# Optimization experiments

Measured on AMD Instinct MI355X. Metric: run time of the kernel, lower is better.

## Reference

```python
import jax, jax.numpy as jnp
import numpy as np

NUM_GENES = 50000
NUM_EDGES = 5000
NNZ = 1_600_000
NUM_PATHWAYS = 500
NUM_TREATMENTS = 20
D = 128        # embed_dim
LATENT = 128   # latent_dim
B, M = 64, 200


def setup_inputs() -> dict:
    key = jax.random.key(0)
    ks = jax.random.split(key, 14)
    gene_ids = jax.random.randint(ks[0], (B, M), 0, NUM_GENES)
    context_ids = jax.random.randint(ks[1], (B,), 0, NUM_TREATMENTS)
    # sparse incidence H (COO): H[row, col] = val, shape [NUM_GENES, NUM_EDGES]
    H_rows = jax.random.randint(ks[2], (NNZ,), 0, NUM_GENES)
    H_cols = jax.random.randint(ks[3], (NNZ,), 0, NUM_EDGES)
    H_vals = jnp.ones((NNZ,), jnp.float32)
    gene_embed = 0.02 * jax.random.normal(ks[4], (NUM_GENES, D), jnp.float32)
    treatment_embed = 0.02 * jax.random.normal(ks[5], (NUM_TREATMENTS, D), jnp.float32)
    gene_pathway = jax.random.bernoulli(ks[6], 0.05, (NUM_GENES, NUM_PATHWAYS)).astype(jnp.float32)
    s = 1.0 / np.sqrt(2 * D)
    W1 = s * jax.random.normal(ks[7], (2 * D, D), jnp.float32)
    b1 = jnp.zeros((D,), jnp.float32)
    W2 = (1.0 / np.sqrt(D)) * jax.random.normal(ks[8], (D,), jnp.float32)
    b2 = jnp.zeros((), jnp.float32)
    latent_W = (1.0 / np.sqrt(D)) * jax.random.normal(ks[9], (D, LATENT), jnp.float32)
    latent_b = jnp.zeros((LATENT,), jnp.float32)
    risk_W = (1.0 / np.sqrt(LATENT)) * jax.random.normal(ks[10], (LATENT,), jnp.float32)
    risk_b = jnp.zeros((), jnp.float32)
    return dict(gene_ids=gene_ids, context_ids=context_ids, H_rows=H_rows, H_cols=H_cols,
                H_vals=H_vals, gene_embed=gene_embed, treatment_embed=treatment_embed,
                gene_pathway=gene_pathway, W1=W1, b1=b1, W2=W2, b2=b2,
                latent_W=latent_W, latent_b=latent_b, risk_W=risk_W, risk_b=risk_b)


def _hyper_prop(E, H_rows, H_cols, H_vals):
    Dv = jax.ops.segment_sum(H_vals, H_rows, num_segments=NUM_GENES)
    De = jax.ops.segment_sum(H_vals, H_cols, num_segments=NUM_EDGES)
    dv = jnp.power(Dv + 1e-6, -0.5)[:, None]   # [V,1]
    de = jnp.power(De + 1e-6, -1.0)[:, None]   # [E,1]
    X = E * dv
    # H^T X : scatter node rows into hyperedges
    HX = jax.ops.segment_sum(H_vals[:, None] * X[H_rows], H_cols, num_segments=NUM_EDGES)
    HX = HX * de
    # H (De^-1 H^T X)
    Xp = jax.ops.segment_sum(H_vals[:, None] * HX[H_cols], H_rows, num_segments=NUM_GENES)
    return Xp * dv


def reference(gene_ids, context_ids, H_rows, H_cols, H_vals, gene_embed, treatment_embed,
              gene_pathway, W1, b1, W2, b2, latent_W, latent_b, risk_W, risk_b):
    E_prop = _hyper_prop(gene_embed, H_rows, H_cols, H_vals)   # [V,D]
    X = E_prop[gene_ids]                                       # [B,M,D]
    ctx = treatment_embed[context_ids]                         # [B,D]
    masks = gene_pathway[gene_ids]                             # [B,M,P]
    pathway_sum = jnp.einsum('bmd,bmp->bpd', X, masks)         # [B,P,D]
    counts = jnp.clip(masks.sum(axis=1), 1.0)[..., None]       # [B,P,1]
    rep = pathway_sum / counts                                 # [B,P,D]
    ctx_exp = jnp.broadcast_to(ctx[:, None, :], (rep.shape[0], NUM_PATHWAYS, D))
    attn_in = jnp.concatenate([rep, ctx_exp], axis=-1)         # [B,P,2D]
    h = jnp.tanh(attn_in @ W1 + b1)                            # [B,P,D]
    scores = h @ W2 + b2                                       # [B,P]
    w = jax.nn.softmax(scores, axis=-1)
    z0 = jnp.einsum('bp,bpd->bd', w, rep)                      # [B,D]
    z = z0 @ latent_W + latent_b                               # [B,LATENT]
    risk = z @ risk_W + risk_b                                 # [B]
    return risk, z
```

## Files before the change

kernel.cpp:

```cpp
#include <hip/hip_runtime.h>
#include <math.h>

#define NGENES 50000
#define NEDGES 5000
#define NNZ_C 1600000
#define NPATH 500
#define DIM 128
#define BB 64
#define MM 200
#define BMN (BB * MM)
#define NBMW 1568
#define CSRCAP 400000
#define NCH 128
#define CHUNK (NNZ_C / NCH)
#define RNG 12512
#define GSTRIDE 50048
#define NT 8
#define TILESZ 6250
#define NBIN (NT * NEDGES)
#define BIN0 50048
#define RED_N 90048
#define SCB_BIN 40
#define SCB_ROW 49
#define SCB (SCB_BIN + SCB_ROW)


__device__ inline float wred_sum(float x) {
#pragma unroll
  for (int off = 32; off > 0; off >>= 1) x += __shfl_down(x, off, 64);
  return x;
}
__device__ inline int wred_sumi(int x) {
#pragma unroll
  for (int off = 32; off > 0; off >>= 1) x += __shfl_down(x, off, 64);
  return x;
}
__device__ inline float wred_max(float x) {
#pragma unroll
  for (int off = 32; off > 0; off >>= 1) x = fmaxf(x, __shfl_down(x, off, 64));
  return x;
}
__device__ inline int wave_incl_scan(int x) {
  int lane = threadIdx.x & 63;
#pragma unroll
  for (int off = 1; off < 64; off <<= 1) {
    int y = __shfl_up(x, off, 64);
    if (lane >= off) x += y;
  }
  return x;
}

__global__ void k_mark(const int* __restrict__ gene_ids, unsigned* __restrict__ bitmap) {
  int i = blockIdx.x * blockDim.x + threadIdx.x;
  if (i >= BMN) return;
  int g = gene_ids[i];
  atomicOr(bitmap + (g >> 5), 1u << (g & 31));
}

__global__ void k_build(const int* __restrict__ rows, const int* __restrict__ cols,
                        unsigned char* __restrict__ pgc, unsigned char* __restrict__ pbc) {
  __shared__ int hs[RNG];
  int c = blockIdx.x, role = blockIdx.y, tid = threadIdx.x;
  int lo = c * CHUNK, hi = lo + CHUNK;
  if (role == 0) {
    for (int j = tid; j < RNG; j += 1024) hs[j] = 0;
    __syncthreads();
    for (int i = lo + tid; i < hi; i += 1024) {
      int r = rows[i];
      int k = r / RNG;
      int j = r - k * RNG;
      atomicAdd(&hs[j], 1 << (k * 8));
    }
    __syncthreads();
    unsigned char* dst = pgc + (size_t)c * GSTRIDE;
    for (int j = tid; j < RNG; j += 1024) {
      unsigned v = (unsigned)hs[j];
      dst[j] = (unsigned char)(v & 0xFFu);
      dst[j + RNG] = (unsigned char)((v >> 8) & 0xFFu);
      dst[j + 2 * RNG] = (unsigned char)((v >> 16) & 0xFFu);
      dst[j + 3 * RNG] = (unsigned char)(v >> 24);
    }
  } else {
    for (int j = tid; j < 2 * NEDGES; j += 1024) hs[j] = 0;
    __syncthreads();
    for (int i = lo + tid; i < hi; i += 1024) {
      int r = rows[i];
      int t = r / TILESZ;
      int e = cols[i];
      atomicAdd(&hs[(t >> 2) * NEDGES + e], 1 << ((t & 3) * 8));
    }
    __syncthreads();
    unsigned char* dst = pbc + (size_t)c * NBIN;
    for (int j = tid; j < 2 * NEDGES; j += 1024) {
      int h = j / NEDGES, e = j - h * NEDGES;
      unsigned v = (unsigned)hs[j];
      int t0 = h * 4;
      dst[(size_t)(t0 + 0) * NEDGES + e] = (unsigned char)(v & 0xFFu);
      dst[(size_t)(t0 + 1) * NEDGES + e] = (unsigned char)((v >> 8) & 0xFFu);
      dst[(size_t)(t0 + 2) * NEDGES + e] = (unsigned char)((v >> 16) & 0xFFu);
      dst[(size_t)(t0 + 3) * NEDGES + e] = (unsigned char)(v >> 24);
    }
  }
}

__global__ void k_reduce(const unsigned char* __restrict__ pgc,
                         const unsigned char* __restrict__ pbc,
                         const unsigned* __restrict__ bitmap,
                         float* __restrict__ dv_inv, int* __restrict__ row_cnt,
                         unsigned short* __restrict__ ccpre8, int* __restrict__ cnt8em) {
  int idx = blockIdx.x * 256 + threadIdx.x;
  if (idx < NGENES) {
    int s = 0;
    for (int c = 0; c < NCH; ++c) s += pgc[(size_t)c * GSTRIDE + idx];
    dv_inv[idx] = 1.f / sqrtf((float)s + 1e-6f);
    row_cnt[idx] = ((bitmap[idx >> 5] >> (idx & 31)) & 1) ? s : 0;
  } else if (idx >= BIN0 && idx < BIN0 + NBIN) {
    int b = idx - BIN0;
    int t = b / NEDGES, e = b - t * NEDGES;
    int run = 0;
    for (int c = 0; c < NCH; ++c) {
      ccpre8[(size_t)c * NBIN + b] = (unsigned short)run;
      run += pbc[(size_t)c * NBIN + b];
    }
    cnt8em[(e << 3) | t] = run;
  }
}

__global__ void k_sc1(const int* __restrict__ cnt8em, const int* __restrict__ row_cnt,
                      int* __restrict__ bsum) {
  __shared__ int wsum[4];
  int blk = blockIdx.x, t = threadIdx.x, lane = t & 63, wid = t >> 6;
  const int* in;
  int base, n;
  if (blk < SCB_BIN) { in = cnt8em; base = blk * 1024; n = NBIN; }
  else { in = row_cnt; base = (blk - SCB_BIN) * 1024; n = NGENES; }
  int s = 0;
#pragma unroll
  for (int k = 0; k < 4; ++k) {
    int e = base + t + k * 256;
    if (e < n) s += in[e];
  }
  s = wred_sumi(s);
  if (lane == 0) wsum[wid] = s;
  __syncthreads();
  if (t == 0) bsum[blk] = wsum[0] + wsum[1] + wsum[2] + wsum[3];
}

__global__ void k_sc2(const int* __restrict__ bsum, int* __restrict__ boff) {
  int t = threadIdx.x, lane = t & 63, wid = t >> 6;
  if (wid == 0) {
    int x = (lane < SCB_BIN) ? bsum[lane] : 0;
    int incl = wave_incl_scan(x);
    if (lane < SCB_BIN) boff[lane] = incl - x;
  } else {
    int x = (lane < SCB_ROW) ? bsum[SCB_BIN + lane] : 0;
    int incl = wave_incl_scan(x);
    if (lane < SCB_ROW) boff[SCB_BIN + lane] = incl - x;
  }
}

__global__ void k_sc3(const int* __restrict__ cnt8em, const int* __restrict__ row_cnt,
                      const int* __restrict__ boff,
                      int* __restrict__ start8, int* __restrict__ row_start,
                      float* __restrict__ de_inv) {
  __shared__ int lds[1024];
  __shared__ int wsum[4];
  int blk = blockIdx.x, t = threadIdx.x, lane = t & 63, wid = t >> 6;
  const int* in;
  int* out;
  int base, n;
  if (blk < SCB_BIN) { in = cnt8em; out = start8; base = blk * 1024; n = NBIN; }
  else { in = row_cnt; out = row_start; base = (blk - SCB_BIN) * 1024; n = NGENES; }
  int coff = boff[blk];
#pragma unroll
  for (int k = 0; k < 4; ++k) {
    int e = t + k * 256;
    lds[e] = (base + e < n) ? in[base + e] : 0;
  }
  __syncthreads();
  int x0 = lds[4 * t], x1 = lds[4 * t + 1], x2 = lds[4 * t + 2], x3 = lds[4 * t + 3];
  int s = x0 + x1 + x2 + x3;
  int incl = wave_incl_scan(s);
  if (lane == 63) wsum[wid] = incl;
  __syncthreads();
  int woff = 0;
  for (int w = 0; w < wid; ++w) woff += wsum[w];
  int tb = coff + woff + incl - s;
  int i0 = base + 4 * t;
  if (i0 + 3 < n) {
    ((int4*)(out + i0))[0] = make_int4(tb, tb + x0, tb + x0 + x1, tb + x0 + x1 + x2);
  } else {
    if (i0 < n) out[i0] = tb;
    if (i0 + 1 < n) out[i0 + 1] = tb + x0;
    if (i0 + 2 < n) out[i0 + 2] = tb + x0 + x1;
    if (i0 + 3 < n) out[i0 + 3] = tb + x0 + x1 + x2;
  }
  if (blk < SCB_BIN && t < 128) {
    int e = blk * 128 + t;
    if (e < NEDGES) {
      int s8 = 0;
#pragma unroll
      for (int u = 0; u < 8; ++u) s8 += lds[8 * t + u];
      de_inv[e] = 1.f / ((float)s8 + 1e-6f);
    }
  }
}

__global__ void k_place(const int* __restrict__ rows, const int* __restrict__ cols,
                        const int* __restrict__ start8, const unsigned short* __restrict__ ccpre8,
                        const int* __restrict__ row_start, int* __restrict__ row_cur,
                        const unsigned* __restrict__ bitmap,
                        unsigned short* __restrict__ csc, unsigned short* __restrict__ csr) {
  __shared__ int cnt_s[NEDGES];
  __shared__ unsigned bm_s[NBMW];
  int c = blockIdx.x, q = blockIdx.y, tid = threadIdx.x;
  int lo = c * CHUNK, hi = lo + CHUNK;
  for (int j = tid; j < NEDGES; j += 1024) cnt_s[j] = 0;
  for (int j = tid; j < NBMW; j += 1024) bm_s[j] = bitmap[j];
  __syncthreads();
  const unsigned short* cp = ccpre8 + (size_t)c * NBIN;
  int qlo = q * (4 * TILESZ);
  for (int i = lo + tid; i < hi; i += 1024) {
    int r = rows[i];
    unsigned d = (unsigned)(r - qlo);
    if (d >= 4u * TILESZ) continue;
    int e = cols[i];
    int tt = (int)(d / (unsigned)TILESZ);
    int t = 4 * q + tt;
    int sh = tt * 8;
    int old = atomicAdd(&cnt_s[e], 1 << sh);
    int rank = (old >> sh) & 0xFF;
    int pos = start8[e * 8 + t] + (int)cp[(size_t)t * NEDGES + e] + rank;
    csc[pos] = (unsigned short)(d - (unsigned)(tt * TILESZ));
    if ((bm_s[r >> 5] >> (r & 31)) & 1) {
      int p2 = row_start[r] + atomicAdd(row_cur + r, 1);
      if (p2 < CSRCAP) csr[p2] = (unsigned short)e;
    }
  }
}

__global__ void k_edge_t(const int* __restrict__ start8, const int* __restrict__ cnt8em,
                         const unsigned short* __restrict__ csc,
                         const float* __restrict__ dv_inv, const float* __restrict__ ge,
                         float* __restrict__ part) {
  __shared__ float4 red[32];
  int bid = blockIdx.x;
  int s = start8[bid];
  int n = cnt8em[bid];
  int rbase = (bid & 7) * TILESZ;
  int g = threadIdx.x >> 5, l = threadIdx.x & 31;
  float4 a0 = make_float4(0.f, 0.f, 0.f, 0.f);
  float4 a1 = make_float4(0.f, 0.f, 0.f, 0.f);
  float4 a2 = make_float4(0.f, 0.f, 0.f, 0.f);
  float4 a3 = make_float4(0.f, 0.f, 0.f, 0.f);
  int i = s + g;
  int end = s + n;
  unsigned short c0 = 0, c1 = 0, c2 = 0, c3 = 0, c4 = 0, c5 = 0, c6 = 0, c7 = 0;
  bool have = (i + 14 < end);
  if (have) {
    c0 = csc[i];      c1 = csc[i + 2];  c2 = csc[i + 4];  c3 = csc[i + 6];
    c4 = csc[i + 8];  c5 = csc[i + 10]; c6 = csc[i + 12]; c7 = csc[i + 14];
  }
  while (have) {
    int ni = i + 16;
    bool nhave = (ni + 14 < end);
    unsigned short n0 = c0, n1 = c1, n2 = c2, n3 = c3, n4 = c4, n5 = c5, n6 = c6, n7 = c7;
    if (nhave) {
      n0 = csc[ni];      n1 = csc[ni + 2];  n2 = csc[ni + 4];  n3 = csc[ni + 6];
      n4 = csc[ni + 8];  n5 = csc[ni + 10]; n6 = csc[ni + 12]; n7 = csc[ni + 14];
    }
    int r0 = rbase + c0, r1 = rbase + c1, r2 = rbase + c2, r3 = rbase + c3;
    int r4 = rbase + c4, r5 = rbase + c5, r6 = rbase + c6, r7 = rbase + c7;
    float w0 = dv_inv[r0], w1 = dv_inv[r1], w2 = dv_inv[r2], w3 = dv_inv[r3];
    float w4 = dv_inv[r4], w5 = dv_inv[r5], w6 = dv_inv[r6], w7 = dv_inv[r7];
    float4 x0 = *((const float4*)(ge + (size_t)r0 * DIM) + l);
    float4 x1 = *((const float4*)(ge + (size_t)r1 * DIM) + l);
    float4 x2 = *((const float4*)(ge + (size_t)r2 * DIM) + l);
    float4 x3 = *((const float4*)(ge + (size_t)r3 * DIM) + l);
    float4 x4 = *((const float4*)(ge + (size_t)r4 * DIM) + l);
    float4 x5 = *((const float4*)(ge + (size_t)r5 * DIM) + l);
    float4 x6 = *((const float4*)(ge + (size_t)r6 * DIM) + l);
    float4 x7 = *((const float4*)(ge + (size_t)r7 * DIM) + l);
    a0.x += w0 * x0.x; a0.y += w0 * x0.y; a0.z += w0 * x0.z; a0.w += w0 * x0.w;
    a1.x += w1 * x1.x; a1.y += w1 * x1.y; a1.z += w1 * x1.z; a1.w += w1 * x1.w;
    a2.x += w2 * x2.x; a2.y += w2 * x2.y; a2.z += w2 * x2.z; a2.w += w2 * x2.w;
    a3.x += w3 * x3.x; a3.y += w3 * x3.y; a3.z += w3 * x3.z; a3.w += w3 * x3.w;
    a0.x += w4 * x4.x; a0.y += w4 * x4.y; a0.z += w4 * x4.z; a0.w += w4 * x4.w;
    a1.x += w5 * x5.x; a1.y += w5 * x5.y; a1.z += w5 * x5.z; a1.w += w5 * x5.w;
    a2.x += w6 * x6.x; a2.y += w6 * x6.y; a2.z += w6 * x6.z; a2.w += w6 * x6.w;
    a3.x += w7 * x7.x; a3.y += w7 * x7.y; a3.z += w7 * x7.z; a3.w += w7 * x7.w;
    c0 = n0; c1 = n1; c2 = n2; c3 = n3; c4 = n4; c5 = n5; c6 = n6; c7 = n7;
    i = ni;
    have = nhave;
  }
  for (; i + 2 < end; i += 4) {
    int ra = rbase + csc[i], rb = rbase + csc[i + 2];
    float wa = dv_inv[ra], wb = dv_inv[rb];
    float4 xa = *((const float4*)(ge + (size_t)ra * DIM) + l);
    float4 xb = *((const float4*)(ge + (size_t)rb * DIM) + l);
    a0.x += wa * xa.x; a0.y += wa * xa.y; a0.z += wa * xa.z; a0.w += wa * xa.w;
    a1.x += wb * xb.x; a1.y += wb * xb.y; a1.z += wb * xb.z; a1.w += wb * xb.w;
  }
  for (; i < end; i += 2) {
    int r = rbase + csc[i];
    float w = dv_inv[r];
    float4 x = *((const float4*)(ge + (size_t)r * DIM) + l);
    a0.x += w * x.x; a0.y += w * x.y; a0.z += w * x.z; a0.w += w * x.w;
  }
  a0.x += a1.x + a2.x + a3.x;
  a0.y += a1.y + a2.y + a3.y;
  a0.z += a1.z + a2.z + a3.z;
  a0.w += a1.w + a2.w + a3.w;
  if (g == 1) red[l] = a0;
  __syncthreads();
  if (g == 0) {
    float4 b = red[l];
    a0.x += b.x; a0.y += b.y; a0.z += b.z; a0.w += b.w;
    *((float4*)(part + (size_t)bid * DIM) + l) = a0;
  }
}

__global__ void k_edge_red(const float* __restrict__ part, const float* __restrict__ de_inv,
                           float* __restrict__ HXde) {
  int e = blockIdx.x, d = threadIdx.x;
  float s = 0.f;
#pragma unroll
  for (int t = 0; t < NT; ++t) s += part[((size_t)e * 8 + t) * DIM + d];
  HXde[(size_t)e * DIM + d] = s * de_inv[e];
}

__global__ void k_gene(const int* __restrict__ gene_ids, const int* __restrict__ row_start,
                       const int* __restrict__ row_cnt, const unsigned short* __restrict__ csr,
                       const float* __restrict__ HXde, const float* __restrict__ dv_inv,
                       float* __restrict__ Xg) {
  __shared__ float4 red[4][32];
  int bm = blockIdx.x;
  int gene = gene_ids[bm];
  int s = row_start[gene], n = row_cnt[gene];
  int end = s + n;
  int g = threadIdx.x >> 5, l = threadIdx.x & 31;
  float4 a0 = make_float4(0.f, 0.f, 0.f, 0.f);
  float4 a1 = make_float4(0.f, 0.f, 0.f, 0.f);
  int i = s + g;
  for (; i + 12 < end; i += 16) {
    int e0 = csr[i];
    int e1 = csr[i + 4];
    int e2 = csr[i + 8];
    int e3 = csr[i + 12];
    float4 x0 = *((const float4*)(HXde + (size_t)e0 * DIM) + l);
    float4 x1 = *((const float4*)(HXde + (size_t)e1 * DIM) + l);
    float4 x2 = *((const float4*)(HXde + (size_t)e2 * DIM) + l);
    float4 x3 = *((const float4*)(HXde + (size_t)e3 * DIM) + l);
    a0.x += x0.x; a0.y += x0.y; a0.z += x0.z; a0.w += x0.w;
    a1.x += x1.x; a1.y += x1.y; a1.z += x1.z; a1.w += x1.w;
    a0.x += x2.x; a0.y += x2.y; a0.z += x2.z; a0.w += x2.w;
    a1.x += x3.x; a1.y += x3.y; a1.z += x3.z; a1.w += x3.w;
  }
  for (; i + 4 < end; i += 8) {
    int e0 = csr[i];
    int e1 = csr[i + 4];
    float4 x0 = *((const float4*)(HXde + (size_t)e0 * DIM) + l);
    float4 x1 = *((const float4*)(HXde + (size_t)e1 * DIM) + l);
    a0.x += x0.x; a0.y += x0.y; a0.z += x0.z; a0.w += x0.w;
    a1.x += x1.x; a1.y += x1.y; a1.z += x1.z; a1.w += x1.w;
  }
  for (; i < end; i += 4) {
    int e0 = csr[i];
    float4 x = *((const float4*)(HXde + (size_t)e0 * DIM) + l);
    a0.x += x.x; a0.y += x.y; a0.z += x.z; a0.w += x.w;
  }
  a0.x += a1.x; a0.y += a1.y; a0.z += a1.z; a0.w += a1.w;
  red[g][l] = a0;
  __syncthreads();
  if (g == 0) {
    float4 a = red[0][l], b = red[1][l], c = red[2][l], d = red[3][l];
    float dvg = dv_inv[gene];
    float4 o;
    o.x = (a.x + b.x + c.x + d.x) * dvg;
    o.y = (a.y + b.y + c.y + d.y) * dvg;
    o.z = (a.z + b.z + c.z + d.z) * dvg;
    o.w = (a.w + b.w + c.w + d.w) * dvg;
    *((float4*)(Xg + (size_t)bm * DIM) + l) = o;
  }
}

#define PT 20
#define CHM 25
__global__ void k_pathway(const int* __restrict__ gene_ids,
                          const float* __restrict__ gene_pathway,
                          const float* __restrict__ Xg, float* __restrict__ rep) {
  __shared__ __align__(16) float buf[2][CHM * PT];
  __shared__ int gid_s[MM];
  __shared__ float cnt_sh[PT];
  int b = blockIdx.y;
  int p0 = blockIdx.x * PT;
  int t = threadIdx.x;
  int d = t;
  if (t < 128) gid_s[t] = gene_ids[b * MM + t];
  if (t + 128 < MM) gid_s[t + 128] = gene_ids[b * MM + t + 128];
  __syncthreads();
  float acc[PT];
#pragma unroll
  for (int pp = 0; pp < PT; ++pp) acc[pp] = 0.f;
  float cntloc = 0.f;
  float r[4];
#pragma unroll
  for (int k = 0; k < 4; ++k) {
    int e = t + k * 128;
    if (e < CHM * PT) {
      int ml = e / PT, po = e - ml * PT;
      r[k] = gene_pathway[(size_t)gid_s[ml] * NPATH + p0 + po];
    }
  }
  const float* Xb = Xg + (size_t)b * MM * DIM + d;
  for (int ch = 0; ch < MM / CHM; ++ch) {
    float* bw = buf[ch & 1];
#pragma unroll
    for (int k = 0; k < 4; ++k) {
      int e = t + k * 128;
      if (e < CHM * PT) bw[e] = r[k];
    }
    __syncthreads();
    if (ch + 1 < MM / CHM) {
      int m0n = (ch + 1) * CHM;
#pragma unroll
      for (int k = 0; k < 4; ++k) {
        int e = t + k * 128;
        if (e < CHM * PT) {
          int ml = e / PT, po = e - ml * PT;
          r[k] = gene_pathway[(size_t)gid_s[m0n + ml] * NPATH + p0 + po];
        }
      }
    }
    const float* br = buf[ch & 1];
    if (t < PT) {
      for (int ml = 0; ml < CHM; ++ml) cntloc += br[ml * PT + t];
    }
    int m0 = ch * CHM;
    for (int ml = 0; ml < CHM; ++ml) {
      float x = Xb[(size_t)(m0 + ml) * DIM];
      const float4* mr = (const float4*)(br + ml * PT);
#pragma unroll
      for (int q = 0; q < 5; ++q) {
        float4 v = mr[q];
        acc[4 * q + 0] += v.x * x;
        acc[4 * q + 1] += v.y * x;
        acc[4 * q + 2] += v.z * x;
        acc[4 * q + 3] += v.w * x;
      }
    }
  }
  if (t < PT) cnt_sh[t] = cntloc;
  __syncthreads();
#pragma unroll
  for (int pp = 0; pp < PT; ++pp) {
    rep[((size_t)b * NPATH + p0 + pp) * DIM + d] = acc[pp] / fmaxf(cnt_sh[pp], 1.f);
  }
}

#define PT2 10
__global__ void k_attn(const float* __restrict__ rep, const int* __restrict__ context_ids,
                       const float* __restrict__ treatment_embed,
                       const float* __restrict__ W1, const float* __restrict__ b1,
                       const float* __restrict__ W2, const float* __restrict__ b2,
                       float* __restrict__ scores) {
  __shared__ float in_s[PT2][DIM];
  __shared__ float ctx_s[DIM];
  __shared__ float part[PT2][2];
  int b = blockIdx.y;
  int p0 = blockIdx.x * PT2;
  int j = threadIdx.x;
  int lane = j & 63, wid = j >> 6;
  ctx_s[j] = treatment_embed[context_ids[b] * DIM + j];
#pragma unroll
  for (int pp = 0; pp < PT2; ++pp)
    in_s[pp][j] = rep[((size_t)b * NPATH + p0 + pp) * DIM + j];
  __syncthreads();
  float base = b1[j];
  for (int k = 0; k < DIM; ++k) base += ctx_s[k] * W1[(DIM + k) * DIM + j];
  float acc[PT2];
#pragma unroll
  for (int pp = 0; pp < PT2; ++pp) acc[pp] = base;
  for (int k = 0; k < DIM; ++k) {
    float w1 = W1[k * DIM + j];
#pragma unroll
    for (int pp = 0; pp < PT2; ++pp) acc[pp] += in_s[pp][k] * w1;
  }
  float w2 = W2[j];
#pragma unroll
  for (int pp = 0; pp < PT2; ++pp) {
    float t = tanhf(acc[pp]) * w2;
    t = wred_sum(t);
    if (lane == 0) part[pp][wid] = t;
  }
  __syncthreads();
  if (j < PT2) scores[b * NPATH + p0 + j] = part[j][0] + part[j][1] + b2[0];
}

__global__ void k_final(const float* __restrict__ scores, const float* __restrict__ rep,
                        const float* __restrict__ latent_W, const float* __restrict__ latent_b,
                        const float* __restrict__ risk_W, const float* __restrict__ risk_b,
                        float* __restrict__ out) {
  __shared__ float w_s[NPATH];
  __shared__ float z0_s[DIM];
  __shared__ float red_max[2], red_sum[2], red_risk[2];
  int b = blockIdx.x, t = threadIdx.x;
  int lane = t & 63, wid = t >> 6;
  float lmax = -3.4e38f;
  for (int p = t; p < NPATH; p += 128) {
    float s = scores[b * NPATH + p];
    w_s[p] = s;
    lmax = fmaxf(lmax, s);
  }
  lmax = wred_max(lmax);
  if (lane == 0) red_max[wid] = lmax;
  __syncthreads();
  float bmax = fmaxf(red_max[0], red_max[1]);
  float lsum = 0.f;
  for (int p = t; p < NPATH; p += 128) {
    float e = expf(w_s[p] - bmax);
    w_s[p] = e;
    lsum += e;
  }
  lsum = wred_sum(lsum);
  if (lane == 0) red_sum[wid] = lsum;
  __syncthreads();
  float inv = 1.f / (red_sum[0] + red_sum[1]);
  int d = t;
  const float* repb = rep + (size_t)b * NPATH * DIM + d;
  float z00 = 0.f, z01 = 0.f, z02 = 0.f, z03 = 0.f;
  for (int p = 0; p < NPATH; p += 4) {
    z00 += w_s[p] * repb[(size_t)p * DIM];
    z01 += w_s[p + 1] * repb[(size_t)(p + 1) * DIM];
    z02 += w_s[p + 2] * repb[(size_t)(p + 2) * DIM];
    z03 += w_s[p + 3] * repb[(size_t)(p + 3) * DIM];
  }
  float z0 = ((z00 + z01) + (z02 + z03)) * inv;
  z0_s[d] = z0;
  __syncthreads();
  float z = latent_b[t];
  for (int dd = 0; dd < DIM; ++dd) z += z0_s[dd] * latent_W[dd * DIM + t];
  out[BB + b * DIM + t] = z;
  float r = z * risk_W[t];
  r = wred_sum(r);
  if (lane == 0) red_risk[wid] = r;
  __syncthreads();
  if (t == 0) out[b] = red_risk[0] + red_risk[1] + risk_b[0];
}

extern "C" void kernel_launch(void* const* d_in, const int* in_sizes, int n_in,
                              void* d_out, int out_size, void* d_ws, size_t ws_size,
                              hipStream_t stream) {
  const int* gene_ids = (const int*)d_in[0];
  const int* context_ids = (const int*)d_in[1];
  const int* H_rows = (const int*)d_in[2];
  const int* H_cols = (const int*)d_in[3];
  const float* gene_embed = (const float*)d_in[5];
  const float* treatment_embed = (const float*)d_in[6];
  const float* gene_pathway = (const float*)d_in[7];
  const float* W1 = (const float*)d_in[8];
  const float* b1 = (const float*)d_in[9];
  const float* W2 = (const float*)d_in[10];
  const float* b2 = (const float*)d_in[11];
  const float* latent_W = (const float*)d_in[12];
  const float* latent_b = (const float*)d_in[13];
  const float* risk_W = (const float*)d_in[14];
  const float* risk_b = (const float*)d_in[15];
  float* out = (float*)d_out;

  char* ws = (char*)d_ws;
  float* dv_inv = (float*)(ws + 0);
  float* de_inv = (float*)(ws + 200000);
  int* row_cnt = (int*)(ws + 220000);
  int* row_start = (int*)(ws + 420000);
  int* cnt8em = (int*)(ws + 620000);
  int* start8 = (int*)(ws + 780000);
  float* scores = (float*)(ws + 940000);
  int* bsum = (int*)(ws + 1068032);
  int* boff = (int*)(ws + 1068544);
  int* row_cur = (int*)(ws + 1069056);
  unsigned* bitmap = (unsigned*)(ws + 1269056);
  unsigned short* ccpre8 = (unsigned short*)(ws + 1275328);
  unsigned char* pgc = (unsigned char*)(ws + 11515328);
  unsigned char* pbc = (unsigned char*)(ws + 17921472);
  unsigned short* csc = (unsigned short*)(ws + 11515328);
  unsigned short* csr = (unsigned short*)(ws + 14715328);
  float* part = (float*)(ws + 15515328);
  float* HXde = (float*)(ws + 11515328);
  float* Xg = (float*)(ws + 15515328);
  float* rep = (float*)(ws + 22068928);

  hipMemsetAsync(ws + 1069056, 0, 206272, stream);

  k_mark<<<(BMN + 255) / 256, 256, 0, stream>>>(gene_ids, bitmap);
  k_build<<<dim3(NCH, 2), 1024, 0, stream>>>(H_rows, H_cols, pgc, pbc);
  k_reduce<<<(RED_N + 255) / 256, 256, 0, stream>>>(pgc, pbc, bitmap, dv_inv, row_cnt,
                                                    ccpre8, cnt8em);
  k_sc1<<<SCB, 256, 0, stream>>>(cnt8em, row_cnt, bsum);
  k_sc2<<<1, 128, 0, stream>>>(bsum, boff);
  k_sc3<<<SCB, 256, 0, stream>>>(cnt8em, row_cnt, boff, start8, row_start, de_inv);
  k_place<<<dim3(NCH, 2), 1024, 0, stream>>>(H_rows, H_cols, start8, ccpre8,
                                             row_start, row_cur, bitmap, csc, csr);
  k_edge_t<<<NBIN, 64, 0, stream>>>(start8, cnt8em, csc, dv_inv, gene_embed, part);
  k_edge_red<<<NEDGES, DIM, 0, stream>>>(part, de_inv, HXde);
  k_gene<<<BMN, 128, 0, stream>>>(gene_ids, row_start, row_cnt, csr, HXde, dv_inv, Xg);
  k_pathway<<<dim3(NPATH / PT, BB), DIM, 0, stream>>>(gene_ids, gene_pathway, Xg, rep);
  k_attn<<<dim3(NPATH / PT2, BB), DIM, 0, stream>>>(rep, context_ids, treatment_embed,
                                                    W1, b1, W2, b2, scores);
  k_final<<<BB, DIM, 0, stream>>>(scores, rep, latent_W, latent_b, risk_W, risk_b, out);
}
```

Before: 410.1 us.

## Fold gene marking into build, hoist context projection, widen attn and final kernels

Removes the separate k_mark launch by marking the gene bitmap inside k_build's first role. The per-batch context half of the W1 projection is computed once in extra k_sc2 blocks, instead of being recomputed in every k_attn block. k_attn now processes 20 pathways per block instead of 10, and k_final uses 256 threads so the weighted sum over pathways and the latent matmul are split across two halves. The goal is fewer launches and less redundant work, at the cost of fewer attn blocks and more register pressure there.

New measurement: 416.7 us. No clear change (+1.6%).

```diff
diff --git a/kernel.cpp b/kernel.cpp
--- a/kernel.cpp
+++ b/kernel.cpp
@@ -50,19 +50,17 @@
   return x;
 }
 
-__global__ void k_mark(const int* __restrict__ gene_ids, unsigned* __restrict__ bitmap) {
-  int i = blockIdx.x * blockDim.x + threadIdx.x;
-  if (i >= BMN) return;
-  int g = gene_ids[i];
-  atomicOr(bitmap + (g >> 5), 1u << (g & 31));
-}
-
 __global__ void k_build(const int* __restrict__ rows, const int* __restrict__ cols,
+                        const int* __restrict__ gene_ids, unsigned* __restrict__ bitmap,
                         unsigned char* __restrict__ pgc, unsigned char* __restrict__ pbc) {
   __shared__ int hs[RNG];
   int c = blockIdx.x, role = blockIdx.y, tid = threadIdx.x;
   int lo = c * CHUNK, hi = lo + CHUNK;
   if (role == 0) {
+    if (tid < 100) {
+      int g = gene_ids[c * 100 + tid];
+      atomicOr(bitmap + (g >> 5), 1u << (g & 31));
+    }
     for (int j = tid; j < RNG; j += 1024) hs[j] = 0;
     __syncthreads();
     for (int i = lo + tid; i < hi; i += 1024) {
@@ -146,16 +144,31 @@
   if (t == 0) bsum[blk] = wsum[0] + wsum[1] + wsum[2] + wsum[3];
 }
 
-__global__ void k_sc2(const int* __restrict__ bsum, int* __restrict__ boff) {
-  int t = threadIdx.x, lane = t & 63, wid = t >> 6;
-  if (wid == 0) {
-    int x = (lane < SCB_BIN) ? bsum[lane] : 0;
-    int incl = wave_incl_scan(x);
-    if (lane < SCB_BIN) boff[lane] = incl - x;
+__global__ void k_sc2(const int* __restrict__ bsum, int* __restrict__ boff,
+                      const int* __restrict__ context_ids,
+                      const float* __restrict__ treatment_embed,
+                      const float* __restrict__ W1, const float* __restrict__ b1,
+                      float* __restrict__ ctxw) {
+  if (blockIdx.x == 0) {
+    int t = threadIdx.x, lane = t & 63, wid = t >> 6;
+    if (wid == 0) {
+      int x = (lane < SCB_BIN) ? bsum[lane] : 0;
+      int incl = wave_incl_scan(x);
+      if (lane < SCB_BIN) boff[lane] = incl - x;
+    } else {
+      int x = (lane < SCB_ROW) ? bsum[SCB_BIN + lane] : 0;
+      int incl = wave_incl_scan(x);
+      if (lane < SCB_ROW) boff[SCB_BIN + lane] = incl - x;
+    }
   } else {
-    int x = (lane < SCB_ROW) ? bsum[SCB_BIN + lane] : 0;
-    int incl = wave_incl_scan(x);
-    if (lane < SCB_ROW) boff[SCB_BIN + lane] = incl - x;
+    __shared__ float ctx_s[DIM];
+    int b = blockIdx.x - 1;
+    int j = threadIdx.x;
+    ctx_s[j] = treatment_embed[context_ids[b] * DIM + j];
+    __syncthreads();
+    float acc = b1[j];
+    for (int k = 0; k < DIM; ++k) acc += ctx_s[k] * W1[(DIM + k) * DIM + j];
+    ctxw[b * DIM + j] = acc;
   }
 }
 
@@ -458,26 +471,21 @@
   }
 }
 
-#define PT2 10
-__global__ void k_attn(const float* __restrict__ rep, const int* __restrict__ context_ids,
-                       const float* __restrict__ treatment_embed,
-                       const float* __restrict__ W1, const float* __restrict__ b1,
-                       const float* __restrict__ W2, const float* __restrict__ b2,
-                       float* __restrict__ scores) {
+#define PT2 20
+__global__ void k_attn(const float* __restrict__ rep, const float* __restrict__ ctxw,
+                       const float* __restrict__ W1, const float* __restrict__ W2,
+                       const float* __restrict__ b2, float* __restrict__ scores) {
   __shared__ float in_s[PT2][DIM];
-  __shared__ float ctx_s[DIM];
   __shared__ float part[PT2][2];
   int b = blockIdx.y;
   int p0 = blockIdx.x * PT2;
   int j = threadIdx.x;
   int lane = j & 63, wid = j >> 6;
-  ctx_s[j] = treatment_embed[context_ids[b] * DIM + j];
 #pragma unroll
   for (int pp = 0; pp < PT2; ++pp)
     in_s[pp][j] = rep[((size_t)b * NPATH + p0 + pp) * DIM + j];
   __syncthreads();
-  float base = b1[j];
-  for (int k = 0; k < DIM; ++k) base += ctx_s[k] * W1[(DIM + k) * DIM + j];
+  float base = ctxw[b * DIM + j];
   float acc[PT2];
 #pragma unroll
   for (int pp = 0; pp < PT2; ++pp) acc[pp] = base;
@@ -502,12 +510,14 @@
                         const float* __restrict__ risk_W, const float* __restrict__ risk_b,
                         float* __restrict__ out) {
   __shared__ float w_s[NPATH];
+  __shared__ float z0h[2][DIM];
+  __shared__ float zh[2][DIM];
   __shared__ float z0_s[DIM];
-  __shared__ float red_max[2], red_sum[2], red_risk[2];
+  __shared__ float red_max[4], red_sum[4], red_risk[2];
   int b = blockIdx.x, t = threadIdx.x;
   int lane = t & 63, wid = t >> 6;
   float lmax = -3.4e38f;
-  for (int p = t; p < NPATH; p += 128) {
+  for (int p = t; p < NPATH; p += 256) {
     float s = scores[b * NPATH + p];
     w_s[p] = s;
     lmax = fmaxf(lmax, s);
@@ -515,9 +525,9 @@
   lmax = wred_max(lmax);
   if (lane == 0) red_max[wid] = lmax;
   __syncthreads();
-  float bmax = fmaxf(red_max[0], red_max[1]);
+  float bmax = fmaxf(fmaxf(red_max[0], red_max[1]), fmaxf(red_max[2], red_max[3]));
   float lsum = 0.f;
-  for (int p = t; p < NPATH; p += 128) {
+  for (int p = t; p < NPATH; p += 256) {
     float e = expf(w_s[p] - bmax);
     w_s[p] = e;
     lsum += e;
@@ -525,25 +535,32 @@
   lsum = wred_sum(lsum);
   if (lane == 0) red_sum[wid] = lsum;
   __syncthreads();
-  float inv = 1.f / (red_sum[0] + red_sum[1]);
-  int d = t;
+  float inv = 1.f / (red_sum[0] + red_sum[1] + red_sum[2] + red_sum[3]);
+  int d = t & 127, half = t >> 7;
   const float* repb = rep + (size_t)b * NPATH * DIM + d;
-  float z00 = 0.f, z01 = 0.f, z02 = 0.f, z03 = 0.f;
-  for (int p = 0; p < NPATH; p += 4) {
-    z00 += w_s[p] * repb[(size_t)p * DIM];
-    z01 += w_s[p + 1] * repb[(size_t)(p + 1) * DIM];
-    z02 += w_s[p + 2] * repb[(size_t)(p + 2) * DIM];
-    z03 += w_s[p + 3] * repb[(size_t)(p + 3) * DIM];
-  }
-  float z0 = ((z00 + z01) + (z02 + z03)) * inv;
-  z0_s[d] = z0;
-  __syncthreads();
-  float z = latent_b[t];
-  for (int dd = 0; dd < DIM; ++dd) z += z0_s[dd] * latent_W[dd * DIM + t];
-  out[BB + b * DIM + t] = z;
-  float r = z * risk_W[t];
-  r = wred_sum(r);
-  if (lane == 0) red_risk[wid] = r;
+  float za = 0.f, zb = 0.f;
+  for (int k = 0; k < 250; k += 2) {
+    int p1 = 2 * k + half;
+    int p2 = p1 + 2;
+    za += w_s[p1] * repb[(size_t)p1 * DIM];
+    zb += w_s[p2] * repb[(size_t)p2 * DIM];
+  }
+  z0h[half][d] = za + zb;
+  __syncthreads();
+  if (half == 0) z0_s[d] = (z0h[0][d] + z0h[1][d]) * inv;
+  __syncthreads();
+  float zp = 0.f;
+  int dd0 = half * 64;
+  for (int dd = dd0; dd < dd0 + 64; ++dd) zp += z0_s[dd] * latent_W[dd * DIM + d];
+  zh[half][d] = zp;
+  __syncthreads();
+  if (half == 0) {
+    float z = latent_b[d] + zh[0][d] + zh[1][d];
+    out[BB + b * DIM + d] = z;
+    float r = z * risk_W[d];
+    r = wred_sum(r);
+    if (lane == 0) red_risk[wid] = r;
+  }
   __syncthreads();
   if (t == 0) out[b] = red_risk[0] + red_risk[1] + risk_b[0];
 }
@@ -578,26 +595,27 @@
   float* scores = (float*)(ws + 940000);
   int* bsum = (int*)(ws + 1068032);
   int* boff = (int*)(ws + 1068544);
-  int* row_cur = (int*)(ws + 1069056);
-  unsigned* bitmap = (unsigned*)(ws + 1269056);
-  unsigned short* ccpre8 = (unsigned short*)(ws + 1275328);
-  unsigned char* pgc = (unsigned char*)(ws + 11515328);
-  unsigned char* pbc = (unsigned char*)(ws + 17921472);
-  unsigned short* csc = (unsigned short*)(ws + 11515328);
-  unsigned short* csr = (unsigned short*)(ws + 14715328);
-  float* part = (float*)(ws + 15515328);
-  float* HXde = (float*)(ws + 11515328);
-  float* Xg = (float*)(ws + 15515328);
-  float* rep = (float*)(ws + 22068928);
-
-  hipMemsetAsync(ws + 1069056, 0, 206272, stream);
-
-  k_mark<<<(BMN + 255) / 256, 256, 0, stream>>>(gene_ids, bitmap);
-  k_build<<<dim3(NCH, 2), 1024, 0, stream>>>(H_rows, H_cols, pgc, pbc);
+  float* ctxw = (float*)(ws + 1069056);
+  int* row_cur = (int*)(ws + 1101824);
+  unsigned* bitmap = (unsigned*)(ws + 1301824);
+  unsigned short* ccpre8 = (unsigned short*)(ws + 1308096);
+  unsigned char* pgc = (unsigned char*)(ws + 11548096);
+  unsigned char* pbc = (unsigned char*)(ws + 17954240);
+  unsigned short* csc = (unsigned short*)(ws + 11548096);
+  unsigned short* csr = (unsigned short*)(ws + 14748096);
+  float* part = (float*)(ws + 15548096);
+  float* HXde = (float*)(ws + 11548096);
+  float* Xg = (float*)(ws + 15548096);
+  float* rep = (float*)(ws + 22101696);
+
+  hipMemsetAsync(ws + 1101824, 0, 206272, stream);
+
+  k_build<<<dim3(NCH, 2), 1024, 0, stream>>>(H_rows, H_cols, gene_ids, bitmap, pgc, pbc);
   k_reduce<<<(RED_N + 255) / 256, 256, 0, stream>>>(pgc, pbc, bitmap, dv_inv, row_cnt,
                                                     ccpre8, cnt8em);
   k_sc1<<<SCB, 256, 0, stream>>>(cnt8em, row_cnt, bsum);
-  k_sc2<<<1, 128, 0, stream>>>(bsum, boff);
+  k_sc2<<<1 + BB, 128, 0, stream>>>(bsum, boff, context_ids, treatment_embed,
+                                    W1, b1, ctxw);
   k_sc3<<<SCB, 256, 0, stream>>>(cnt8em, row_cnt, boff, start8, row_start, de_inv);
   k_place<<<dim3(NCH, 2), 1024, 0, stream>>>(H_rows, H_cols, start8, ccpre8,
                                              row_start, row_cur, bitmap, csc, csr);
@@ -605,7 +623,6 @@
   k_edge_red<<<NEDGES, DIM, 0, stream>>>(part, de_inv, HXde);
   k_gene<<<BMN, 128, 0, stream>>>(gene_ids, row_start, row_cnt, csr, HXde, dv_inv, Xg);
   k_pathway<<<dim3(NPATH / PT, BB), DIM, 0, stream>>>(gene_ids, gene_pathway, Xg, rep);
-  k_attn<<<dim3(NPATH / PT2, BB), DIM, 0, stream>>>(rep, context_ids, treatment_embed,
-                                                    W1, b1, W2, b2, scores);
-  k_final<<<BB, DIM, 0, stream>>>(scores, rep, latent_W, latent_b, risk_W, risk_b, out);
-}
+  k_attn<<<dim3(NPATH / PT2, BB), DIM, 0, stream>>>(rep, ctxw, W1, W2, b2, scores);
+  k_final<<<BB, 256, 0, stream>>>(scores, rep, latent_W, latent_b, risk_W, risk_b, out);
+}
```
